# Optimization experiments

Hardware: AMD Instinct MI355X
Metric: run time of the kernel (lower is better)

## Reference

```python
import jax, jax.numpy as jnp
import numpy as np
from jax import lax

B, S, E, H, V = 32, 128, 512, 512, 32000


def setup_inputs() -> dict:
    key = jax.random.key(0)
    ks = jax.random.split(key, 12)
    s = 1.0 / np.sqrt(H)
    u = lambda k, shape: jax.random.uniform(k, shape, jnp.float32, -s, s)
    return {
        "inputs": jax.random.randint(ks[0], (B, S), 0, V, dtype=jnp.int32),
        "encoder_outputs": jax.random.normal(ks[1], (B, S, H), jnp.float32),
        "lengths": jnp.full((B,), S, dtype=jnp.int32),
        "h0": jnp.zeros((B, H), jnp.float32),
        "c0": jnp.zeros((B, H), jnp.float32),
        "emb": jax.random.normal(ks[2], (V, E), jnp.float32) * 0.02,
        "W_ih": u(ks[3], (4 * H, E)),
        "W_hh": u(ks[4], (4 * H, H)),
        "b_ih": u(ks[5], (4 * H,)),
        "b_hh": u(ks[6], (4 * H,)),
        "W_out": u(ks[7], (V, H)),
        "b_out": u(ks[8], (V,)),
    }


def _decode(inputs, h0, c0, emb, W_ih, W_hh, b_ih, b_hh, W_out, b_out):
    # Teacher-forced per-step LSTM decode. PyTorch LSTM gate order: i, f, g, o.
    def step(carry, tok):
        h, c = carry                              # [B, H] each
        x = emb[tok]                              # [B, E] embedding lookup
        gates = x @ W_ih.T + b_ih + h @ W_hh.T + b_hh  # [B, 4H]
        i, f, g, o = jnp.split(gates, 4, axis=-1)
        i = jax.nn.sigmoid(i)
        f = jax.nn.sigmoid(f)
        g = jnp.tanh(g)
        o = jax.nn.sigmoid(o)
        c = f * c + i * g
        h = o * jnp.tanh(c)
        logp = jax.nn.log_softmax(h @ W_out.T + b_out, axis=-1)  # [B, V]
        # NLLLoss (mean over batch) against the same step's input token,
        # exactly as the original forward computes it.
        nll = -jnp.take_along_axis(logp, tok[:, None], axis=-1).mean()
        sym = jnp.argmax(logp, axis=-1)           # topk(1) indices
        return (h, c), (nll, sym)

    (_, _), (losses, syms) = lax.scan(step, (h0, c0), inputs.T)  # scan over S
    return losses.sum(), syms.T                   # scalar, [B, S]


def reference(inputs, encoder_outputs, lengths, h0, c0, emb,
              W_ih, W_hh, b_ih, b_hh, W_out, b_out):
    # encoder_outputs / lengths are unused (attention is None; lengths[0] == S).
    loss, symbols = _decode(inputs, h0, c0, emb, W_ih, W_hh, b_ih, b_hh, W_out, b_out)
    return loss, symbols
```

## Files before the change

kernel.cpp:

```cpp
#include <hip/hip_runtime.h>
#include <math.h>

#define B_ 32
#define S_ 128
#define H_ 512
#define V_ 32000
#define G4_ 2048
#define NGB 250
#define RBLK 64

typedef __attribute__((ext_vector_type(8))) short bf8;
typedef __attribute__((ext_vector_type(4))) float f4;
typedef unsigned short us;

__device__ __forceinline__ us f2bf(float x) {
    union { float f; unsigned u; } v; v.f = x;
    unsigned r = v.u + 0x7FFFu + ((v.u >> 16) & 1u);
    return (us)(r >> 16);
}
__device__ __forceinline__ float bf2f(us b) {
    union { unsigned u; float f; } v; v.u = ((unsigned)b) << 16; return v.f;
}
__device__ __forceinline__ float4 ldf4(const float* p) {
    return *reinterpret_cast<const float4*>(p);
}
__device__ __forceinline__ void gload_lds16(const void* g, void* l) {
    __builtin_amdgcn_global_load_lds((const __attribute__((address_space(1))) unsigned*)g,
                                     (__attribute__((address_space(3))) unsigned*)l, 16, 0, 0);
}

__global__ __launch_bounds__(256) void k_whh3(const float* __restrict__ W,
                                              us* __restrict__ B1,
                                              us* __restrict__ B2,
                                              us* __restrict__ B3) {
    const size_t id = (size_t)blockIdx.x * 256 + threadIdx.x;
    const int lane = (int)(id & 63);
    const size_t fc = id >> 6;
    const int kc = (int)(fc & 15);
    const size_t gt = fc >> 4;
    const int nt = (int)(gt & 1);
    const int g = (int)(gt >> 1);
    const int c = lane & 15;
    const int q = nt * 2 + (c >> 3), nl = c & 7;
    const int row = q * 512 + g * 8 + nl;
    const int k0 = kc * 32 + (lane >> 4) * 8;
    const float* src = W + (size_t)row * H_ + k0;
    bf8 v1, v2, v3;
#pragma unroll
    for (int e = 0; e < 8; ++e) {
        float x = src[e];
        us a1 = f2bf(x);
        float r1 = x - bf2f(a1);
        us a2 = f2bf(r1);
        float r2 = r1 - bf2f(a2);
        v1[e] = (short)a1; v2[e] = (short)a2; v3[e] = (short)f2bf(r2);
    }
    *reinterpret_cast<bf8*>(B1 + id * 8) = v1;
    *reinterpret_cast<bf8*>(B2 + id * 8) = v2;
    *reinterpret_cast<bf8*>(B3 + id * 8) = v3;
}

__global__ __launch_bounds__(256) void k_xw(const int* __restrict__ inputs,
                                            const float* __restrict__ emb,
                                            const float* __restrict__ W_ih,
                                            const float* __restrict__ b_ih,
                                            const float* __restrict__ b_hh,
                                            float* __restrict__ XW) {
    __shared__ float es[16 * H_];
    const int tid = threadIdx.x;
    const int j = blockIdx.x * 256 + tid;
    const int t = blockIdx.y;
    const float bias = b_ih[j] + b_hh[j];
#pragma unroll
    for (int half = 0; half < 2; ++half) {
        __syncthreads();
        for (int idx = tid; idx < 16 * 128; idx += 256) {
            int b = idx >> 7, k4 = (idx & 127) << 2;
            int tok = inputs[(half * 16 + b) * S_ + t];
            *reinterpret_cast<float4*>(&es[b * H_ + k4]) = ldf4(emb + (size_t)tok * H_ + k4);
        }
        __syncthreads();
        float acc[16];
#pragma unroll
        for (int b = 0; b < 16; ++b) acc[b] = 0.f;
        for (int k = 0; k < H_; k += 4) {
            float4 wv = ldf4(W_ih + (size_t)j * H_ + k);
#pragma unroll
            for (int b = 0; b < 16; ++b) {
                float4 xv = *reinterpret_cast<const float4*>(&es[b * H_ + k]);
                acc[b] += wv.x * xv.x + wv.y * xv.y + wv.z * xv.z + wv.w * xv.w;
            }
        }
#pragma unroll
        for (int b = 0; b < 16; ++b)
            XW[(size_t)(t * B_ + half * 16 + b) * G4_ + j] = acc[b] + bias;
    }
}

__global__ __launch_bounds__(256)
void k_recur(const float* __restrict__ h0, const float* __restrict__ c0,
             const us* __restrict__ B1f, const us* __restrict__ B2f,
             const us* __restrict__ B3f, const float* __restrict__ XW,
             us* __restrict__ A1, us* __restrict__ A2,
             us* __restrict__ A3, int* __restrict__ flags) {
    __shared__ us wl1[16384], wl2[16384], wl3[16384];
    __shared__ float glds[32][33];
    const int g = blockIdx.x, tid = threadIdx.x;

    {
        const size_t base = (size_t)g * 16384;
        for (int i = tid; i < 2048; i += 256) {
            reinterpret_cast<uint4*>(wl1)[i] = reinterpret_cast<const uint4*>(B1f + base)[i];
            reinterpret_cast<uint4*>(wl2)[i] = reinterpret_cast<const uint4*>(B2f + base)[i];
            reinterpret_cast<uint4*>(wl3)[i] = reinterpret_cast<const uint4*>(B3f + base)[i];
        }
    }
    const int b = tid >> 3, nl = tid & 7;
    const int n = g * 8 + nl;
    const int kc_w = g >> 2, kg_w = g & 3, half_w = b >> 4, lane_w = kg_w * 16 + (b & 15);
    float c_reg = c0[b * H_ + n];
    float hn = h0[b * H_ + n];

    auto write_frags = [&](int slot, float h) {
        us a1 = f2bf(h);
        float r1 = h - bf2f(a1);
        us a2 = f2bf(r1);
        us a3 = f2bf(r1 - bf2f(a2));
        unsigned v1 = a1, v2 = a2, v3 = a3;
        unsigned q1 = (unsigned)__shfl_xor((int)v1, 1);
        unsigned q2 = (unsigned)__shfl_xor((int)v2, 1);
        unsigned q3 = (unsigned)__shfl_xor((int)v3, 1);
        if ((nl & 1) == 0) {
            const size_t ix = ((((size_t)slot * 16 + kc_w) * 2 + half_w) * 64 + lane_w) * 8 + nl;
            __hip_atomic_store((unsigned*)(A1 + ix), v1 | (q1 << 16),
                               __ATOMIC_RELAXED, __HIP_MEMORY_SCOPE_AGENT);
            __hip_atomic_store((unsigned*)(A2 + ix), v2 | (q2 << 16),
                               __ATOMIC_RELAXED, __HIP_MEMORY_SCOPE_AGENT);
            __hip_atomic_store((unsigned*)(A3 + ix), v3 | (q3 << 16),
                               __ATOMIC_RELAXED, __HIP_MEMORY_SCOPE_AGENT);
        }
    };
    write_frags(0, hn);
    asm volatile("s_waitcnt vmcnt(0)" ::: "memory");
    __syncthreads();
    if (tid == 0)
        __hip_atomic_store(&flags[g * 32], 1, __ATOMIC_RELAXED, __HIP_MEMORY_SCOPE_AGENT);

    const int wv = tid >> 6, lane = tid & 63;
    const int mt = wv >> 1, nt = wv & 1;
    const int cidx = lane & 15;

    for (int t = 0; t < S_; ++t) {
        if (tid < 64) {
            int spins = 0;
            while (__hip_atomic_load(&flags[tid * 32], __ATOMIC_RELAXED,
                                     __HIP_MEMORY_SCOPE_AGENT) < t + 1) {
                __builtin_amdgcn_s_sleep(1);
                if (++spins > (1 << 18)) break;
            }
        }
        __syncthreads();
        f4 acc = {0.f, 0.f, 0.f, 0.f};
        const us* a1p = A1 + ((((size_t)t * 16) * 2 + mt) * 64 + lane) * 8;
        const us* a2p = A2 + ((((size_t)t * 16) * 2 + mt) * 64 + lane) * 8;
        const us* a3p = A3 + ((((size_t)t * 16) * 2 + mt) * 64 + lane) * 8;
        const us* b1p = wl1 + ((size_t)(nt * 16) * 64 + lane) * 8;
        const us* b2p = wl2 + ((size_t)(nt * 16) * 64 + lane) * 8;
        const us* b3p = wl3 + ((size_t)(nt * 16) * 64 + lane) * 8;
#pragma unroll 4
        for (int kc = 0; kc < 16; ++kc) {
            bf8 A1v = *reinterpret_cast<const bf8*>(a1p + (size_t)kc * 1024);
            bf8 A2v = *reinterpret_cast<const bf8*>(a2p + (size_t)kc * 1024);
            bf8 A3v = *reinterpret_cast<const bf8*>(a3p + (size_t)kc * 1024);
            bf8 B1v = *reinterpret_cast<const bf8*>(b1p + (size_t)kc * 512);
            bf8 B2v = *reinterpret_cast<const bf8*>(b2p + (size_t)kc * 512);
            bf8 B3v = *reinterpret_cast<const bf8*>(b3p + (size_t)kc * 512);
            acc = __builtin_amdgcn_mfma_f32_16x16x32_bf16(A1v, B1v, acc, 0, 0, 0);
            acc = __builtin_amdgcn_mfma_f32_16x16x32_bf16(A1v, B2v, acc, 0, 0, 0);
            acc = __builtin_amdgcn_mfma_f32_16x16x32_bf16(A2v, B1v, acc, 0, 0, 0);
            acc = __builtin_amdgcn_mfma_f32_16x16x32_bf16(A2v, B2v, acc, 0, 0, 0);
            acc = __builtin_amdgcn_mfma_f32_16x16x32_bf16(A1v, B3v, acc, 0, 0, 0);
            acc = __builtin_amdgcn_mfma_f32_16x16x32_bf16(A3v, B1v, acc, 0, 0, 0);
        }
#pragma unroll
        for (int r = 0; r < 4; ++r)
            glds[mt * 16 + (lane >> 4) * 4 + r][nt * 16 + cidx] = acc[r];
        __syncthreads();
        const float* xwp = XW + ((size_t)t * B_ + b) * G4_;
        const float s_i = glds[b][nl]      + xwp[0 * 512 + n];
        const float s_f = glds[b][8 + nl]  + xwp[1 * 512 + n];
        const float s_g = glds[b][16 + nl] + xwp[2 * 512 + n];
        const float s_o = glds[b][24 + nl] + xwp[3 * 512 + n];
        const float ig = 1.f / (1.f + expf(-s_i));
        const float fg = 1.f / (1.f + expf(-s_f));
        const float gg = tanhf(s_g);
        const float og = 1.f / (1.f + expf(-s_o));
        c_reg = fg * c_reg + ig * gg;
        hn = og * tanhf(c_reg);
        write_frags(t + 1, hn);
        asm volatile("s_waitcnt vmcnt(0)" ::: "memory");
        __syncthreads();
        if (tid == 0)
            __hip_atomic_store(&flags[g * 32], t + 2, __ATOMIC_RELAXED,
                               __HIP_MEMORY_SCOPE_AGENT);
    }
}

__global__ __launch_bounds__(512, 1) void k_gemm(const int* __restrict__ inputs,
                                                 const us* __restrict__ Ah,
                                                 const us* __restrict__ Al,
                                                 const float* __restrict__ Wout,
                                                 const float* __restrict__ b_out,
                                                 float* __restrict__ sp) {
    __shared__ us abuf[2][32768];
    __shared__ float slds[B_][132];
    const int tid = threadIdx.x;
    const int w = tid >> 6, lane = tid & 63;
    const int vt = blockIdx.x * 8 + w;
    const int v0 = blockIdx.x * 128;
    const int c = lane & 15, kg = lane >> 4;
    const int bb = tid >> 4, sub = tid & 15;

    bf8 Bh[16], Bl[16];
    {
        const float* wrow = Wout + (size_t)(vt * 16 + c) * H_ + kg * 8;
#pragma unroll
        for (int kc = 0; kc < 16; ++kc) {
            const float* src = wrow + kc * 32;
            float4 w0 = ldf4(src), w1 = ldf4(src + 4);
            bf8 hv, lv;
            float xs[8] = {w0.x, w0.y, w0.z, w0.w, w1.x, w1.y, w1.z, w1.w};
#pragma unroll
            for (int e = 0; e < 8; ++e) {
                us hb = f2bf(xs[e]);
                hv[e] = (short)hb;
                lv[e] = (short)f2bf(xs[e] - bf2f(hb));
            }
            Bh[kc] = hv;
            Bl[kc] = lv;
        }
    }
#pragma unroll
    for (int kc = 0; kc < 16; ++kc)
        asm volatile("" : "+v"(Bh[kc]), "+v"(Bl[kc]));

    float bo[8];
#pragma unroll
    for (int q = 0; q < 8; ++q) bo[q] = b_out[v0 + sub * 8 + q];

    auto stage = [&](int slot, int buf) {
        const us* s1 = Ah + (size_t)slot * 16384;
        const us* s2 = Al + (size_t)slot * 16384;
        for (int ch = w; ch < 64; ch += 8) {
            const us* src = (ch < 32 ? s1 + ch * 512 : s2 + (ch - 32) * 512) + lane * 8;
            gload_lds16(src, &abuf[buf][ch * 512]);
        }
    };

    stage(1, 0);
    asm volatile("s_waitcnt vmcnt(0)" ::: "memory");
    __builtin_amdgcn_s_barrier();

    for (int mt = 0; mt < S_; ++mt) {
        const int buf = mt & 1;
        if (mt + 1 < S_) stage(mt + 2, buf ^ 1);
        f4 acc0 = {0.f, 0.f, 0.f, 0.f}, acc1 = {0.f, 0.f, 0.f, 0.f};
#pragma unroll
        for (int kc = 0; kc < 16; ++kc) {
            const int o0 = ((kc * 2 + 0) * 64 + lane) * 8;
            const int o1 = ((kc * 2 + 1) * 64 + lane) * 8;
            bf8 A0h = *reinterpret_cast<const bf8*>(&abuf[buf][o0]);
            bf8 A1h = *reinterpret_cast<const bf8*>(&abuf[buf][o1]);
            bf8 A0l = *reinterpret_cast<const bf8*>(&abuf[buf][16384 + o0]);
            bf8 A1l = *reinterpret_cast<const bf8*>(&abuf[buf][16384 + o1]);
            acc0 = __builtin_amdgcn_mfma_f32_16x16x32_bf16(A0h, Bh[kc], acc0, 0, 0, 0);
            acc1 = __builtin_amdgcn_mfma_f32_16x16x32_bf16(A1h, Bh[kc], acc1, 0, 0, 0);
            acc0 = __builtin_amdgcn_mfma_f32_16x16x32_bf16(A0l, Bh[kc], acc0, 0, 0, 0);
            acc1 = __builtin_amdgcn_mfma_f32_16x16x32_bf16(A1l, Bh[kc], acc1, 0, 0, 0);
            acc0 = __builtin_amdgcn_mfma_f32_16x16x32_bf16(A0h, Bl[kc], acc0, 0, 0, 0);
            acc1 = __builtin_amdgcn_mfma_f32_16x16x32_bf16(A1h, Bl[kc], acc1, 0, 0, 0);
        }
        __builtin_amdgcn_s_barrier();
#pragma unroll
        for (int r = 0; r < 4; ++r) {
            slds[kg * 4 + r][w * 16 + c] = acc0[r];
            slds[16 + kg * 4 + r][w * 16 + c] = acc1[r];
        }
        asm volatile("s_waitcnt lgkmcnt(0)" ::: "memory");
        __builtin_amdgcn_s_barrier();
        const int tok = inputs[bb * S_ + mt];
        float m = -INFINITY, s = 0.f, mv = -INFINITY, tv = -INFINITY;
        int mi = 0x7fffffff;
#pragma unroll
        for (int q = 0; q < 8; ++q) {
            const int vl = sub * 8 + q, v = v0 + vl;
            float x = slds[bb][vl] + bo[q];
            float nm = fmaxf(m, x);
            s = s * __expf(m - nm) + __expf(x - nm);
            m = nm;
            if (x > mv) { mv = x; mi = v; }
            if (v == tok) tv = x;
        }
#pragma unroll
        for (int off = 1; off < 16; off <<= 1) {
            float cm = __shfl_xor(m, off), cs = __shfl_xor(s, off);
            float cmv = __shfl_xor(mv, off), ctv = __shfl_xor(tv, off);
            int cmi = __shfl_xor(mi, off);
            float nm = fmaxf(m, cm);
            s = s * __expf(m - nm) + cs * __expf(cm - nm);
            m = nm;
            if (cmv > mv || (cmv == mv && cmi < mi)) { mv = cmv; mi = cmi; }
            tv = fmaxf(tv, ctv);
        }
        if (sub == 0) {
            float* o = sp + ((size_t)(mt * 32 + bb) * NGB + blockIdx.x) * 5;
            o[0] = m; o[1] = s; o[2] = mv; o[3] = (float)mi; o[4] = tv;
        }
        asm volatile("s_waitcnt vmcnt(0)" ::: "memory");
        __builtin_amdgcn_s_barrier();
    }
}

__global__ __launch_bounds__(256) void k_merge(const float* __restrict__ sp,
                                               float* __restrict__ out,
                                               float* __restrict__ lossbuf,
                                               int* __restrict__ done) {
    const int tid = threadIdx.x;
    const int mi16 = tid >> 4, l16 = tid & 15;
    const int m = blockIdx.x * 16 + mi16;
    float mm = -INFINITY, s = 0.f, mv = -INFINITY, tv = -INFINITY;
    int ai = 0x7fffffff;
    for (int i = l16; i < NGB; i += 16) {
        const float* o = sp + ((size_t)m * NGB + i) * 5;
        float cm = o[0], cs = o[1], cmv = o[2], ctv = o[4];
        int cmi = (int)o[3];
        float nm = fmaxf(mm, cm);
        s = s * expf(mm - nm) + cs * expf(cm - nm);
        mm = nm;
        if (cmv > mv || (cmv == mv && cmi < ai)) { mv = cmv; ai = cmi; }
        tv = fmaxf(tv, ctv);
    }
#pragma unroll
    for (int off = 1; off < 16; off <<= 1) {
        float cm = __shfl_xor(mm, off), cs = __shfl_xor(s, off);
        float cmv = __shfl_xor(mv, off), ctv = __shfl_xor(tv, off);
        int cmi = __shfl_xor(ai, off);
        float nm = fmaxf(mm, cm);
        s = s * expf(mm - nm) + cs * expf(cm - nm);
        mm = nm;
        if (cmv > mv || (cmv == mv && cmi < ai)) { mv = cmv; ai = cmi; }
        tv = fmaxf(tv, ctv);
    }
    if (l16 == 0) {
        const float logZ = mm + logf(s);
        const int t = m >> 5, b = m & 31;
        out[1 + b * S_ + t] = (float)ai;
        lossbuf[m] = tv - logZ;
    }
    __syncthreads();
    __shared__ int lastflag;
    if (tid == 0) {
        __threadfence();
        int prev = __hip_atomic_fetch_add(done, 1, __ATOMIC_ACQ_REL,
                                          __HIP_MEMORY_SCOPE_AGENT);
        lastflag = (prev == (B_ * S_ / 16) - 1) ? 1 : 0;
    }
    __syncthreads();
    if (lastflag) {
        float a = 0.f;
        for (int i = tid; i < B_ * S_; i += 256) a += lossbuf[i];
        __shared__ float red[256];
        red[tid] = a;
        __syncthreads();
        for (int off = 128; off > 0; off >>= 1) {
            if (tid < off) red[tid] += red[tid + off];
            __syncthreads();
        }
        if (tid == 0) out[0] = -red[0] / (float)B_;
    }
}

extern "C" void kernel_launch(void* const* d_in, const int* in_sizes, int n_in,
                              void* d_out, int out_size, void* d_ws, size_t ws_size,
                              hipStream_t stream) {
    const int*   inputs = (const int*)d_in[0];
    const float* h0     = (const float*)d_in[3];
    const float* c0     = (const float*)d_in[4];
    const float* emb    = (const float*)d_in[5];
    const float* W_ih   = (const float*)d_in[6];
    const float* W_hh   = (const float*)d_in[7];
    const float* b_ih   = (const float*)d_in[8];
    const float* b_hh   = (const float*)d_in[9];
    const float* W_out  = (const float*)d_in[10];
    const float* b_out  = (const float*)d_in[11];
    float* out = (float*)d_out;

    char* p = (char*)d_ws;
    auto alloc = [&](size_t bytes) { char* r = p; p += (bytes + 255) & ~255ull; return r; };
    float* lossbuf  = (float*)alloc((size_t)B_ * S_ * 4);
    int*   flags    = (int*)alloc(64 * 32 * 4 + 256);
    float* sp       = (float*)alloc((size_t)B_ * S_ * NGB * 5 * 4);
    us* A1  = (us*)alloc((size_t)(S_ + 1) * 16384 * 2);
    us* A2  = (us*)alloc((size_t)(S_ + 1) * 16384 * 2);
    us* A3  = (us*)alloc((size_t)(S_ + 1) * 16384 * 2);
    us* B1f = (us*)alloc((size_t)RBLK * 16384 * 2);
    us* B2f = (us*)alloc((size_t)RBLK * 16384 * 2);
    us* B3f = (us*)alloc((size_t)RBLK * 16384 * 2);
    float* XW = (float*)alloc((size_t)S_ * B_ * G4_ * 4);
    int* done = flags + 64 * 32;

    (void)hipMemsetAsync(flags, 0, 64 * 32 * 4 + 256, stream);
    k_whh3<<<(RBLK * 2 * 16 * 64) / 256, 256, 0, stream>>>(W_hh, B1f, B2f, B3f);
    k_xw<<<dim3(8, S_), 256, 0, stream>>>(inputs, emb, W_ih, b_ih, b_hh, XW);
    k_recur<<<RBLK, 256, 0, stream>>>(h0, c0, B1f, B2f, B3f, XW, A1, A2, A3, flags);
    k_gemm<<<NGB, 512, 0, stream>>>(inputs, A1, A2, W_out, b_out, sp);
    k_merge<<<(B_ * S_) / 16, 256, 0, stream>>>(sp, out, lossbuf, done);
}
```

Baseline: 1.621 ms.

## Switch output GEMM to 32x32x16 MFMA with 4 waves; vectorize h publish stores

The vocabulary GEMM kernel now uses 4 waves per block, each owning 32 output columns with 32x32x16 bf16 MFMAs and split accumulators, which halves the block size and doubles register-resident W_out fragments. The softmax partial reduction is rebalanced to 16 columns per thread across 8 lanes. In the recurrence, hidden-state fragments are gathered by shuffles into 16-byte stores with cache-bypass bits, replacing many 4-byte atomic stores. The XW loads are also hoisted ahead of the spin-wait so their latency overlaps synchronization. The cost is higher register pressure in the GEMM and reliance on sc0/sc1 store semantics for cross-block visibility.

After: 1.725 ms. 6.4% more time.

```diff
diff --git a/kernel.cpp b/kernel.cpp
--- a/kernel.cpp
+++ b/kernel.cpp
@@ -11,6 +11,8 @@
 
 typedef __attribute__((ext_vector_type(8))) short bf8;
 typedef __attribute__((ext_vector_type(4))) float f4;
+typedef __attribute__((ext_vector_type(16))) float f16x;
+typedef __attribute__((ext_vector_type(4))) unsigned u32x4;
 typedef unsigned short us;
 
 __device__ __forceinline__ us f2bf(float x) {
@@ -27,6 +29,10 @@
 __device__ __forceinline__ void gload_lds16(const void* g, void* l) {
     __builtin_amdgcn_global_load_lds((const __attribute__((address_space(1))) unsigned*)g,
                                      (__attribute__((address_space(3))) unsigned*)l, 16, 0, 0);
+}
+__device__ __forceinline__ void store16_sc(void* gaddr, u32x4 d) {
+    asm volatile("global_store_dwordx4 %0, %1, off sc0 sc1"
+                 :: "v"(gaddr), "v"(d) : "memory");
 }
 
 __global__ __launch_bounds__(256) void k_whh3(const float* __restrict__ W,
@@ -120,27 +126,35 @@
     const int kc_w = g >> 2, kg_w = g & 3, half_w = b >> 4, lane_w = kg_w * 16 + (b & 15);
     float c_reg = c0[b * H_ + n];
     float hn = h0[b * H_ + n];
-
-    auto write_frags = [&](int slot, float h) {
+    const int lane0 = tid & 63;
+    const int lb = lane0 & 56;
+
+    auto publish = [&](int slot, float h) {
         us a1 = f2bf(h);
         float r1 = h - bf2f(a1);
         us a2 = f2bf(r1);
         us a3 = f2bf(r1 - bf2f(a2));
-        unsigned v1 = a1, v2 = a2, v3 = a3;
-        unsigned q1 = (unsigned)__shfl_xor((int)v1, 1);
-        unsigned q2 = (unsigned)__shfl_xor((int)v2, 1);
-        unsigned q3 = (unsigned)__shfl_xor((int)v3, 1);
-        if ((nl & 1) == 0) {
-            const size_t ix = ((((size_t)slot * 16 + kc_w) * 2 + half_w) * 64 + lane_w) * 8 + nl;
-            __hip_atomic_store((unsigned*)(A1 + ix), v1 | (q1 << 16),
-                               __ATOMIC_RELAXED, __HIP_MEMORY_SCOPE_AGENT);
-            __hip_atomic_store((unsigned*)(A2 + ix), v2 | (q2 << 16),
-                               __ATOMIC_RELAXED, __HIP_MEMORY_SCOPE_AGENT);
-            __hip_atomic_store((unsigned*)(A3 + ix), v3 | (q3 << 16),
-                               __ATOMIC_RELAXED, __HIP_MEMORY_SCOPE_AGENT);
+        unsigned p1 = ((unsigned)a1 & 0xffffu) |
+                      (((unsigned)(us)__shfl_xor((int)a1, 1)) << 16);
+        unsigned p2 = ((unsigned)a2 & 0xffffu) |
+                      (((unsigned)(us)__shfl_xor((int)a2, 1)) << 16);
+        unsigned p3 = ((unsigned)a3 & 0xffffu) |
+                      (((unsigned)(us)__shfl_xor((int)a3, 1)) << 16);
+        u32x4 d1, d2, d3;
+        d1[0] = p1; d1[1] = (unsigned)__shfl((int)p1, lb + 2);
+        d1[2] = (unsigned)__shfl((int)p1, lb + 4); d1[3] = (unsigned)__shfl((int)p1, lb + 6);
+        d2[0] = p2; d2[1] = (unsigned)__shfl((int)p2, lb + 2);
+        d2[2] = (unsigned)__shfl((int)p2, lb + 4); d2[3] = (unsigned)__shfl((int)p2, lb + 6);
+        d3[0] = p3; d3[1] = (unsigned)__shfl((int)p3, lb + 2);
+        d3[2] = (unsigned)__shfl((int)p3, lb + 4); d3[3] = (unsigned)__shfl((int)p3, lb + 6);
+        if (nl == 0) {
+            const size_t ix = ((((size_t)slot * 16 + kc_w) * 2 + half_w) * 64 + lane_w) * 8;
+            store16_sc(A1 + ix, d1);
+            store16_sc(A2 + ix, d2);
+            store16_sc(A3 + ix, d3);
         }
     };
-    write_frags(0, hn);
+    publish(0, hn);
     asm volatile("s_waitcnt vmcnt(0)" ::: "memory");
     __syncthreads();
     if (tid == 0)
@@ -151,6 +165,8 @@
     const int cidx = lane & 15;
 
     for (int t = 0; t < S_; ++t) {
+        const float* xwp = XW + ((size_t)t * B_ + b) * G4_;
+        float xw0 = xwp[n], xw1 = xwp[512 + n], xw2 = xwp[1024 + n], xw3 = xwp[1536 + n];
         if (tid < 64) {
             int spins = 0;
             while (__hip_atomic_load(&flags[tid * 32], __ATOMIC_RELAXED,
@@ -186,18 +202,17 @@
         for (int r = 0; r < 4; ++r)
             glds[mt * 16 + (lane >> 4) * 4 + r][nt * 16 + cidx] = acc[r];
         __syncthreads();
-        const float* xwp = XW + ((size_t)t * B_ + b) * G4_;
-        const float s_i = glds[b][nl]      + xwp[0 * 512 + n];
-        const float s_f = glds[b][8 + nl]  + xwp[1 * 512 + n];
-        const float s_g = glds[b][16 + nl] + xwp[2 * 512 + n];
-        const float s_o = glds[b][24 + nl] + xwp[3 * 512 + n];
+        const float s_i = glds[b][nl]      + xw0;
+        const float s_f = glds[b][8 + nl]  + xw1;
+        const float s_g = glds[b][16 + nl] + xw2;
+        const float s_o = glds[b][24 + nl] + xw3;
         const float ig = 1.f / (1.f + expf(-s_i));
         const float fg = 1.f / (1.f + expf(-s_f));
         const float gg = tanhf(s_g);
         const float og = 1.f / (1.f + expf(-s_o));
         c_reg = fg * c_reg + ig * gg;
         hn = og * tanhf(c_reg);
-        write_frags(t + 1, hn);
+        publish(t + 1, hn);
         asm volatile("s_waitcnt vmcnt(0)" ::: "memory");
         __syncthreads();
         if (tid == 0)
@@ -206,7 +221,7 @@
     }
 }
 
-__global__ __launch_bounds__(512, 1) void k_gemm(const int* __restrict__ inputs,
+__global__ __launch_bounds__(256, 1) void k_gemm(const int* __restrict__ inputs,
                                                  const us* __restrict__ Ah,
                                                  const us* __restrict__ Al,
                                                  const float* __restrict__ Wout,
@@ -215,43 +230,44 @@
     __shared__ us abuf[2][32768];
     __shared__ float slds[B_][132];
     const int tid = threadIdx.x;
-    const int w = tid >> 6, lane = tid & 63;
-    const int vt = blockIdx.x * 8 + w;
+    const int wv = tid >> 6, lane = tid & 63;
     const int v0 = blockIdx.x * 128;
-    const int c = lane & 15, kg = lane >> 4;
-    const int bb = tid >> 4, sub = tid & 15;
-
-    bf8 Bh[16], Bl[16];
+    const int col0g = v0 + wv * 32;
+    const int n32 = lane & 31, khalf = lane >> 5;
+    const int chalf = n32 >> 4, c16 = n32 & 15;
+
+    bf8 Bh[32], Bl[32];
     {
-        const float* wrow = Wout + (size_t)(vt * 16 + c) * H_ + kg * 8;
-#pragma unroll
-        for (int kc = 0; kc < 16; ++kc) {
-            const float* src = wrow + kc * 32;
+        const float* wrow = Wout + (size_t)(col0g + n32) * H_ + khalf * 8;
+#pragma unroll
+        for (int kk = 0; kk < 32; ++kk) {
+            const float* src = wrow + kk * 16;
             float4 w0 = ldf4(src), w1 = ldf4(src + 4);
+            float xs[8] = {w0.x, w0.y, w0.z, w0.w, w1.x, w1.y, w1.z, w1.w};
             bf8 hv, lv;
-            float xs[8] = {w0.x, w0.y, w0.z, w0.w, w1.x, w1.y, w1.z, w1.w};
 #pragma unroll
             for (int e = 0; e < 8; ++e) {
                 us hb = f2bf(xs[e]);
                 hv[e] = (short)hb;
                 lv[e] = (short)f2bf(xs[e] - bf2f(hb));
             }
-            Bh[kc] = hv;
-            Bl[kc] = lv;
-        }
-    }
-#pragma unroll
-    for (int kc = 0; kc < 16; ++kc)
-        asm volatile("" : "+v"(Bh[kc]), "+v"(Bl[kc]));
-
-    float bo[8];
-#pragma unroll
-    for (int q = 0; q < 8; ++q) bo[q] = b_out[v0 + sub * 8 + q];
+            Bh[kk] = hv;
+            Bl[kk] = lv;
+        }
+    }
+#pragma unroll
+    for (int kk = 0; kk < 32; ++kk)
+        asm volatile("" : "+v"(Bh[kk]), "+v"(Bl[kk]));
+
+    const int bb = tid >> 3, sub = tid & 7;
+    float bo[16];
+#pragma unroll
+    for (int q = 0; q < 16; ++q) bo[q] = b_out[v0 + sub * 16 + q];
 
     auto stage = [&](int slot, int buf) {
         const us* s1 = Ah + (size_t)slot * 16384;
         const us* s2 = Al + (size_t)slot * 16384;
-        for (int ch = w; ch < 64; ch += 8) {
+        for (int ch = wv; ch < 64; ch += 4) {
             const us* src = (ch < 32 ? s1 + ch * 512 : s2 + (ch - 32) * 512) + lane * 8;
             gload_lds16(src, &abuf[buf][ch * 512]);
         }
@@ -264,27 +280,24 @@
     for (int mt = 0; mt < S_; ++mt) {
         const int buf = mt & 1;
         if (mt + 1 < S_) stage(mt + 2, buf ^ 1);
-        f4 acc0 = {0.f, 0.f, 0.f, 0.f}, acc1 = {0.f, 0.f, 0.f, 0.f};
-#pragma unroll
-        for (int kc = 0; kc < 16; ++kc) {
-            const int o0 = ((kc * 2 + 0) * 64 + lane) * 8;
-            const int o1 = ((kc * 2 + 1) * 64 + lane) * 8;
-            bf8 A0h = *reinterpret_cast<const bf8*>(&abuf[buf][o0]);
-            bf8 A1h = *reinterpret_cast<const bf8*>(&abuf[buf][o1]);
-            bf8 A0l = *reinterpret_cast<const bf8*>(&abuf[buf][16384 + o0]);
-            bf8 A1l = *reinterpret_cast<const bf8*>(&abuf[buf][16384 + o1]);
-            acc0 = __builtin_amdgcn_mfma_f32_16x16x32_bf16(A0h, Bh[kc], acc0, 0, 0, 0);
-            acc1 = __builtin_amdgcn_mfma_f32_16x16x32_bf16(A1h, Bh[kc], acc1, 0, 0, 0);
-            acc0 = __builtin_amdgcn_mfma_f32_16x16x32_bf16(A0l, Bh[kc], acc0, 0, 0, 0);
-            acc1 = __builtin_amdgcn_mfma_f32_16x16x32_bf16(A1l, Bh[kc], acc1, 0, 0, 0);
-            acc0 = __builtin_amdgcn_mfma_f32_16x16x32_bf16(A0h, Bl[kc], acc0, 0, 0, 0);
-            acc1 = __builtin_amdgcn_mfma_f32_16x16x32_bf16(A1h, Bl[kc], acc1, 0, 0, 0);
-        }
+        f16x accA = {0.f,0.f,0.f,0.f,0.f,0.f,0.f,0.f,0.f,0.f,0.f,0.f,0.f,0.f,0.f,0.f};
+        f16x accB = {0.f,0.f,0.f,0.f,0.f,0.f,0.f,0.f,0.f,0.f,0.f,0.f,0.f,0.f,0.f,0.f};
+#pragma unroll
+        for (int kk = 0; kk < 32; ++kk) {
+            const int ofs = (((kk >> 1) * 2 + chalf) * 64 +
+                             (((kk & 1) << 1) + khalf) * 16 + c16) * 8;
+            bf8 Avh = *reinterpret_cast<const bf8*>(&abuf[buf][ofs]);
+            bf8 Avl = *reinterpret_cast<const bf8*>(&abuf[buf][16384 + ofs]);
+            accA = __builtin_amdgcn_mfma_f32_32x32x16_bf16(Avh, Bh[kk], accA, 0, 0, 0);
+            accB = __builtin_amdgcn_mfma_f32_32x32x16_bf16(Avl, Bh[kk], accB, 0, 0, 0);
+            accA = __builtin_amdgcn_mfma_f32_32x32x16_bf16(Avh, Bl[kk], accA, 0, 0, 0);
+        }
+        f16x acc = accA + accB;
         __builtin_amdgcn_s_barrier();
 #pragma unroll
-        for (int r = 0; r < 4; ++r) {
-            slds[kg * 4 + r][w * 16 + c] = acc0[r];
-            slds[16 + kg * 4 + r][w * 16 + c] = acc1[r];
+        for (int r = 0; r < 16; ++r) {
+            const int row = (r & 3) + 8 * (r >> 2) + 4 * khalf;
+            slds[row][wv * 32 + n32] = acc[r];
         }
         asm volatile("s_waitcnt lgkmcnt(0)" ::: "memory");
         __builtin_amdgcn_s_barrier();
@@ -292,8 +305,8 @@
         float m = -INFINITY, s = 0.f, mv = -INFINITY, tv = -INFINITY;
         int mi = 0x7fffffff;
 #pragma unroll
-        for (int q = 0; q < 8; ++q) {
-            const int vl = sub * 8 + q, v = v0 + vl;
+        for (int q = 0; q < 16; ++q) {
+            const int vl = sub * 16 + q, v = v0 + vl;
             float x = slds[bb][vl] + bo[q];
             float nm = fmaxf(m, x);
             s = s * __expf(m - nm) + __expf(x - nm);
@@ -302,7 +315,7 @@
             if (v == tok) tv = x;
         }
 #pragma unroll
-        for (int off = 1; off < 16; off <<= 1) {
+        for (int off = 1; off < 8; off <<= 1) {
             float cm = __shfl_xor(m, off), cs = __shfl_xor(s, off);
             float cmv = __shfl_xor(mv, off), ctv = __shfl_xor(tv, off);
             int cmi = __shfl_xor(mi, off);
@@ -413,6 +426,6 @@
     k_whh3<<<(RBLK * 2 * 16 * 64) / 256, 256, 0, stream>>>(W_hh, B1f, B2f, B3f);
     k_xw<<<dim3(8, S_), 256, 0, stream>>>(inputs, emb, W_ih, b_ih, b_hh, XW);
     k_recur<<<RBLK, 256, 0, stream>>>(h0, c0, B1f, B2f, B3f, XW, A1, A2, A3, flags);
-    k_gemm<<<NGB, 512, 0, stream>>>(inputs, A1, A2, W_out, b_out, sp);
+    k_gemm<<<NGB, 256, 0, stream>>>(inputs, A1, A2, W_out, b_out, sp);
     k_merge<<<(B_ * S_) / 16, 256, 0, stream>>>(sp, out, lossbuf, done);
 }
```
